# Optimization experiments

Measured on AMD Instinct MI355X. Metric: run time of the kernel, lower is better.

## Reference

```python
import jax, jax.numpy as jnp
import numpy as np

B, D, E, H, T = 16384, 32, 8, 64, 10  # batch, state_dim, n_experts, hidden, time points
TEMP = 1.0  # gating temperature


def setup_inputs() -> dict:
    key = jax.random.key(0)
    ks = jax.random.split(key, 12)
    w = lambda k, shape, fan_in: (jax.random.normal(k, shape, jnp.float32) / np.sqrt(fan_in)).astype(jnp.float32)
    return {
        "x0": jax.random.normal(ks[0], (B, D), jnp.float32),
        "t_span": jnp.linspace(0.0, 1.0, T).astype(jnp.float32),
        # per-expert time-conditioned MLP: (x, t) -> H -> H -> D
        "W1": w(ks[1], (E, D + 1, H), D + 1), "b1": jnp.zeros((E, H), jnp.float32),
        "W2": w(ks[2], (E, H, H), H),          "b2": jnp.zeros((E, H), jnp.float32),
        "W3": w(ks[3], (E, H, D), H),          "b3": jnp.zeros((E, D), jnp.float32),
        # gating MLP on concat(x, dx_init): 2D -> H -> E
        "Gw1": w(ks[4], (2 * D, H), 2 * D), "Gb1": jnp.zeros((H,), jnp.float32),
        "Gw2": w(ks[5], (H, E), H),         "Gb2": jnp.zeros((E,), jnp.float32),
    }


def _dyn(t, x, W1, b1, W2, b2, W3, b3, Gw1, Gb1, Gw2, Gb2):
    # AME-ODE training-path dynamics: uniform-weighted init, gate, weighted sum
    inp = jnp.concatenate([x, jnp.ones((x.shape[0], 1), x.dtype) * t], axis=-1)  # [B, D+1]
    h = jnp.tanh(jnp.einsum('bi,eih->beh', inp, W1) + b1)
    h = jnp.tanh(jnp.einsum('beh,ehg->beg', h, W2) + b2)
    f = jnp.einsum('beg,egd->bed', h, W3) + b3          # all-expert dynamics [B, E, D]
    dx_init = f.mean(axis=1)                             # uniform weights 1/E
    g = jnp.tanh(jnp.concatenate([x, dx_init], -1) @ Gw1 + Gb1)
    wgt = jax.nn.softmax((g @ Gw2 + Gb2) / TEMP, axis=-1)  # [B, E]
    return jnp.einsum('be,bed->bd', wgt, f)


def reference(x0, t_span, W1, b1, W2, b2, W3, b3, Gw1, Gb1, Gw2, Gb2):
    params = (W1, b1, W2, b2, W3, b3, Gw1, Gb1, Gw2, Gb2)

    def step(x, ts):
        t0, t1 = ts[0], ts[1]
        dt = t1 - t0
        k1 = _dyn(t0, x, *params)
        k2 = _dyn(t0 + 0.5 * dt, x + 0.5 * dt * k1, *params)
        k3 = _dyn(t0 + 0.5 * dt, x + 0.5 * dt * k2, *params)
        k4 = _dyn(t1, x + dt * k3, *params)
        xn = x + (dt / 6.0) * (k1 + 2.0 * k2 + 2.0 * k3 + k4)
        return xn, xn

    pairs = jnp.stack([t_span[:-1], t_span[1:]], axis=1)  # [T-1, 2]
    _, traj = jax.lax.scan(step, x0, pairs)               # [T-1, B, D]
    traj = jnp.concatenate([x0[None], traj], axis=0)       # [T, B, D]
    return jnp.transpose(traj, (1, 0, 2))                  # [B, T, D]
```

## Files before the change

kernel.cpp:

```cpp
#include <hip/hip_runtime.h>
#include <hip/hip_bf16.h>

typedef unsigned int u32;
typedef unsigned short u16;
typedef __attribute__((ext_vector_type(8))) short short8;
typedef __attribute__((ext_vector_type(4))) float f32x4;
typedef __attribute__((ext_vector_type(4))) u32 u32x4;
typedef __attribute__((ext_vector_type(2))) u32 u32x2;

#define DD 32
#define EE 8
#define HH 64
#define TT 10
#define BATCH 16384
#define EPB 64
#define DYN_LDS 88064

#if __has_builtin(__builtin_amdgcn_exp2f)
#define EXP2F(x) __builtin_amdgcn_exp2f(x)
#else
#define EXP2F(x) __builtin_exp2f(x)
#endif

__device__ __forceinline__ float fast_tanh(float x) {
  float e = EXP2F(x * 2.885390082f);
  return 1.f - 2.f * __builtin_amdgcn_rcpf(e + 1.f);
}
__device__ __forceinline__ u16 f2b_rn(float v) {
  return (u16)((__float_as_uint(v) + 0x8000u) >> 16);
}
__device__ __forceinline__ u32 pack2_rn(float a, float b) {
  return __builtin_amdgcn_perm(__float_as_uint(b) + 0x8000u,
                               __float_as_uint(a) + 0x8000u, 0x07060302u);
}
__device__ __forceinline__ float unp_lo(u32 p) { return __uint_as_float(p << 16); }
__device__ __forceinline__ float unp_hi(u32 p) { return __uint_as_float(p & 0xffff0000u); }
__device__ __forceinline__ short8 lds_frag(const u32* p) {
  u32x4 v = *(const u32x4*)p;
  return __builtin_bit_cast(short8, v);
}
__device__ __forceinline__ f32x4 bcast4(float v) { f32x4 c; c[0]=v; c[1]=v; c[2]=v; c[3]=v; return c; }

__global__ __launch_bounds__(512) void ame_ode_kernel(
    const float* __restrict__ x0, const float* __restrict__ tspan,
    const float* __restrict__ W1, const float* __restrict__ b1,
    const float* __restrict__ W2, const float* __restrict__ b2,
    const float* __restrict__ W3, const float* __restrict__ b3,
    const float* __restrict__ Gw1, const float* __restrict__ Gb1,
    const float* __restrict__ Gw2, const float* __restrict__ Gb2,
    float* __restrict__ out)
{
  extern __shared__ __align__(16) u32 dynbuf[];
  u32*  const xdb = dynbuf;
  u32*  const fsb = dynbuf + 1280;
  float* const lg = (float*)(dynbuf + 9728);
  u32*  const usb = dynbuf + 10496;
  u32*  const hs  = dynbuf + 12800;

  const int tid  = threadIdx.x;
  const int lane = tid & 63;
  const int l15  = lane & 15;
  const int quad = lane >> 4;
  const int e    = __builtin_amdgcn_readfirstlane(tid >> 6);
  const int b    = blockIdx.x * EPB + lane;

  const float* W1f = W1 + e * (DD + 1) * HH;
  const float* b1f = b1 + e * HH;
  const float* W2f = W2 + e * HH * HH;
  const float* b2f = b2 + e * HH;
  const float* W3f = W3 + e * HH * DD;
  const float* b3f = b3 + e * DD;

  short8 bw1[4], bw2[2][4], bw3[2][2];
  #pragma unroll
  for (int nt = 0; nt < 4; nt++)
    #pragma unroll
    for (int j = 0; j < 8; j++)
      bw1[nt][j] = (short)f2b_rn(W1f[(quad * 8 + j) * HH + nt * 16 + l15]);
  #pragma unroll
  for (int ks = 0; ks < 2; ks++)
    #pragma unroll
    for (int nt = 0; nt < 4; nt++)
      #pragma unroll
      for (int j = 0; j < 8; j++)
        bw2[ks][nt][j] = (short)f2b_rn(W2f[(ks * 32 + quad * 8 + j) * HH + nt * 16 + l15]);
  #pragma unroll
  for (int ks = 0; ks < 2; ks++)
    #pragma unroll
    for (int dt2 = 0; dt2 < 2; dt2++)
      #pragma unroll
      for (int j = 0; j < 8; j++)
        bw3[ks][dt2][j] = (short)f2b_rn(W3f[(ks * 32 + quad * 8 + j) * DD + dt2 * 16 + l15]);

  const int g1mt = e & 3;
  const int g1n0 = (e >> 2) * 2;
  short8 bg1x[2], bg1f[2];
  #pragma unroll
  for (int ni = 0; ni < 2; ni++)
    #pragma unroll
    for (int j = 0; j < 8; j++) {
      bg1x[ni][j] = (short)f2b_rn(Gw1[(quad * 8 + j) * HH + (g1n0 + ni) * 16 + l15]);
      bg1f[ni][j] = (short)f2b_rn(0.125f * Gw1[(DD + quad * 8 + j) * HH + (g1n0 + ni) * 16 + l15]);
    }
  const float gb1a = Gb1[g1n0 * 16 + l15];
  const float gb1b = Gb1[(g1n0 + 1) * 16 + l15];

  short8 bg2[2];
  float gb2v = 0.f;
  if (e < 4) {
    #pragma unroll
    for (int ks = 0; ks < 2; ks++)
      #pragma unroll
      for (int j = 0; j < 8; j++)
        bg2[ks][j] = (short)((l15 < 8) ? f2b_rn(Gw2[(ks * 32 + quad * 8 + j) * EE + l15]) : 0);
    gb2v = (l15 < 8) ? Gb2[l15] : 0.f;
  }

  u32 c1p[4], c2p[2], c3p;
  #pragma unroll
  for (int nt = 0; nt < 4; nt++)
    c1p[nt] = pack2_rn(b1f[nt * 16 + l15], W1f[DD * HH + nt * 16 + l15]);
  #pragma unroll
  for (int p = 0; p < 2; p++)
    c2p[p] = pack2_rn(b2f[(2 * p) * 16 + l15], b2f[(2 * p + 1) * 16 + l15]);
  c3p = pack2_rn(b3f[l15], b3f[16 + l15]);

  float xst[4], xacc[4];
  {
    const float4 v = *(const float4*)(x0 + b * DD + 4 * e);
    xst[0] = v.x; xst[1] = v.y; xst[2] = v.z; xst[3] = v.w;
    xacc[0] = v.x; xacc[1] = v.y; xacc[2] = v.z; xacc[3] = v.w;
    u32x2 p; p.x = pack2_rn(v.x, v.y); p.y = pack2_rn(v.z, v.w);
    *(u32x2*)&xdb[lane * 20 + 2 * e] = p;
    *(float4*)(out + b * TT * DD + 4 * e) = v;
  }
  __syncthreads();

  u16* const fw16 = (u16*)fsb;
  u16* const us16 = (u16*)usb;

  #pragma unroll 1
  for (int step = 0; step < TT - 1; step++) {
    const float t0 = tspan[step];
    const float t1 = tspan[step + 1];
    const float dt = t1 - t0;

    #pragma unroll 1
    for (int s = 0; s < 4; s++) {
      const float tcur = (s == 0) ? t0 : ((s == 3) ? t1 : t0 + 0.5f * dt);

      f32x4 c1i[4];
      #pragma unroll
      for (int nt = 0; nt < 4; nt++)
        c1i[nt] = bcast4(__builtin_fmaf(tcur, unp_hi(c1p[nt]), unp_lo(c1p[nt])));

      #pragma unroll 2
      for (int mt = 0; mt < 4; mt++) {
        u32* const hw   = hs + e * 1152 + (mt & 1) * 576;
        u16* const hw16 = (u16*)hw;

        const short8 a1 = lds_frag(&xdb[(mt * 16 + l15) * 20 + quad * 4]);
        f32x4 h1a[4];
        #pragma unroll
        for (int nt = 0; nt < 4; nt++)
          h1a[nt] = __builtin_amdgcn_mfma_f32_16x16x32_bf16(a1, bw1[nt], c1i[nt], 0, 0, 0);
        #pragma unroll
        for (int nt = 0; nt < 4; nt++)
          #pragma unroll
          for (int r = 0; r < 4; r++)
            hw16[(quad * 4 + r) * 72 + nt * 16 + l15] = f2b_rn(fast_tanh(h1a[nt][r]));

        f32x4 h2a[4];
        #pragma unroll
        for (int nt = 0; nt < 4; nt++)
          h2a[nt] = bcast4((nt & 1) ? unp_hi(c2p[nt >> 1]) : unp_lo(c2p[nt >> 1]));
        #pragma unroll
        for (int ks = 0; ks < 2; ks++) {
          const short8 a2 = lds_frag(&hw[l15 * 36 + ks * 16 + quad * 4]);
          #pragma unroll
          for (int nt = 0; nt < 4; nt++)
            h2a[nt] = __builtin_amdgcn_mfma_f32_16x16x32_bf16(a2, bw2[ks][nt], h2a[nt], 0, 0, 0);
        }
        #pragma unroll
        for (int nt = 0; nt < 4; nt++)
          #pragma unroll
          for (int r = 0; r < 4; r++)
            hw16[(quad * 4 + r) * 72 + nt * 16 + l15] = f2b_rn(fast_tanh(h2a[nt][r]));

        f32x4 fa[2];
        #pragma unroll
        for (int dt2 = 0; dt2 < 2; dt2++)
          fa[dt2] = bcast4(dt2 ? unp_hi(c3p) : unp_lo(c3p));
        #pragma unroll
        for (int ks = 0; ks < 2; ks++) {
          const short8 a3 = lds_frag(&hw[l15 * 36 + ks * 16 + quad * 4]);
          #pragma unroll
          for (int dt2 = 0; dt2 < 2; dt2++)
            fa[dt2] = __builtin_amdgcn_mfma_f32_16x16x32_bf16(a3, bw3[ks][dt2], fa[dt2], 0, 0, 0);
        }
        #pragma unroll
        for (int dt2 = 0; dt2 < 2; dt2++)
          #pragma unroll
          for (int r = 0; r < 4; r++)
            fw16[(mt * 16 + quad * 4 + r) * 264 + e * 32 + dt2 * 16 + l15] = f2b_rn(fa[dt2][r]);
      }
      __syncthreads();

      {
        f32x4 u0 = bcast4(gb1a), u1 = bcast4(gb1b);
        const int mg = g1mt * 16 + l15;
        const short8 ax = lds_frag(&xdb[mg * 20 + quad * 4]);
        u0 = __builtin_amdgcn_mfma_f32_16x16x32_bf16(ax, bg1x[0], u0, 0, 0, 0);
        u1 = __builtin_amdgcn_mfma_f32_16x16x32_bf16(ax, bg1x[1], u1, 0, 0, 0);
        #pragma unroll
        for (int kb = 0; kb < 8; kb++) {
          const short8 af = lds_frag(&fsb[mg * 132 + kb * 16 + quad * 4]);
          u0 = __builtin_amdgcn_mfma_f32_16x16x32_bf16(af, bg1f[0], u0, 0, 0, 0);
          u1 = __builtin_amdgcn_mfma_f32_16x16x32_bf16(af, bg1f[1], u1, 0, 0, 0);
        }
        #pragma unroll
        for (int r = 0; r < 4; r++) {
          us16[(g1mt * 16 + quad * 4 + r) * 72 + g1n0 * 16 + l15]       = f2b_rn(fast_tanh(u0[r]));
          us16[(g1mt * 16 + quad * 4 + r) * 72 + (g1n0 + 1) * 16 + l15] = f2b_rn(fast_tanh(u1[r]));
        }
      }
      __syncthreads();

      if (e < 4) {
        f32x4 lv = bcast4(gb2v);
        #pragma unroll
        for (int ks = 0; ks < 2; ks++) {
          const short8 ag = lds_frag(&usb[(e * 16 + l15) * 36 + ks * 16 + quad * 4]);
          lv = __builtin_amdgcn_mfma_f32_16x16x32_bf16(ag, bg2[ks], lv, 0, 0, 0);
        }
        if (l15 < 8) {
          #pragma unroll
          for (int r = 0; r < 4; r++)
            lg[(e * 16 + quad * 4 + r) * 12 + l15] = lv[r];
        }
      }
      __syncthreads();

      {
        const float4 la0 = *(const float4*)&lg[lane * 12 + 0];
        const float4 la1 = *(const float4*)&lg[lane * 12 + 4];
        float w8[EE];
        w8[0] = __expf(la0.x); w8[1] = __expf(la0.y);
        w8[2] = __expf(la0.z); w8[3] = __expf(la0.w);
        w8[4] = __expf(la1.x); w8[5] = __expf(la1.y);
        w8[6] = __expf(la1.z); w8[7] = __expf(la1.w);
        float ss = 0.f;
        #pragma unroll
        for (int j = 0; j < EE; j++) ss += w8[j];
        const float inv = __builtin_amdgcn_rcpf(ss);

        float kc[4] = {0.f, 0.f, 0.f, 0.f};
        #pragma unroll
        for (int j = 0; j < EE; j++) {
          const float wg = w8[j] * inv;
          const u32x2 p = *(const u32x2*)&fsb[lane * 132 + j * 16 + 2 * e];
          kc[0] = __builtin_fmaf(wg, unp_lo(p.x), kc[0]);
          kc[1] = __builtin_fmaf(wg, unp_hi(p.x), kc[1]);
          kc[2] = __builtin_fmaf(wg, unp_lo(p.y), kc[2]);
          kc[3] = __builtin_fmaf(wg, unp_hi(p.y), kc[3]);
        }

        const float wk = (s == 1 || s == 2) ? 2.f : 1.f;
        const float ak = dt * (1.f / 6.f) * wk;
        #pragma unroll
        for (int q = 0; q < 4; q++) xacc[q] = __builtin_fmaf(ak, kc[q], xacc[q]);

        float xn[4];
        if (s < 3) {
          const float cn = (s == 2) ? dt : 0.5f * dt;
          #pragma unroll
          for (int q = 0; q < 4; q++) xn[q] = __builtin_fmaf(cn, kc[q], xst[q]);
        } else {
          #pragma unroll
          for (int q = 0; q < 4; q++) { xst[q] = xacc[q]; xn[q] = xacc[q]; }
          float4 o; o.x = xn[0]; o.y = xn[1]; o.z = xn[2]; o.w = xn[3];
          *(float4*)(out + (b * TT + step + 1) * DD + 4 * e) = o;
        }
        u32x2 p; p.x = pack2_rn(xn[0], xn[1]); p.y = pack2_rn(xn[2], xn[3]);
        *(u32x2*)&xdb[lane * 20 + 2 * e] = p;
      }
      __syncthreads();
    }
  }
}

extern "C" void kernel_launch(void* const* d_in, const int* in_sizes, int n_in,
                              void* d_out, int out_size, void* d_ws, size_t ws_size,
                              hipStream_t stream)
{
  const float* x0    = (const float*)d_in[0];
  const float* tspan = (const float*)d_in[1];
  const float* W1  = (const float*)d_in[2];
  const float* b1  = (const float*)d_in[3];
  const float* W2  = (const float*)d_in[4];
  const float* b2  = (const float*)d_in[5];
  const float* W3  = (const float*)d_in[6];
  const float* b3  = (const float*)d_in[7];
  const float* Gw1 = (const float*)d_in[8];
  const float* Gb1 = (const float*)d_in[9];
  const float* Gw2 = (const float*)d_in[10];
  const float* Gb2 = (const float*)d_in[11];

  (void)hipFuncSetAttribute((const void*)ame_ode_kernel,
                            hipFuncAttributeMaxDynamicSharedMemorySize, DYN_LDS);

  ame_ode_kernel<<<BATCH / EPB, 512, DYN_LDS, stream>>>(
      x0, tspan, W1, b1, W2, b2, W3, b3, Gw1, Gb1, Gw2, Gb2, (float*)d_out);
}
```

Baseline: 318.4 us.

## Halve batch elements per block to 32 and remap gating and combine work

Reduces the number of batch rows each 512-thread block processes from 64 to 32. This doubles the grid size and shrinks the LDS footprint, so more blocks can be resident on each CU. The gating MLP tiles are remapped so each wave owns one 16x16 output tile, and the combine stage now gives each thread two state elements. Per-block weight loading and bf16 conversion are amortized over half as many rows, and each wave does less MFMA work per barrier, which may expose synchronization overhead.

```diff
diff --git a/kernel.cpp b/kernel.cpp
--- a/kernel.cpp
+++ b/kernel.cpp
@@ -13,8 +13,8 @@
 #define HH 64
 #define TT 10
 #define BATCH 16384
-#define EPB 64
-#define DYN_LDS 88064
+#define EPB 32
+#define DYN_LDS 62464
 
 #if __has_builtin(__builtin_amdgcn_exp2f)
 #define EXP2F(x) __builtin_amdgcn_exp2f(x)
@@ -52,17 +52,20 @@
 {
   extern __shared__ __align__(16) u32 dynbuf[];
   u32*  const xdb = dynbuf;
-  u32*  const fsb = dynbuf + 1280;
-  float* const lg = (float*)(dynbuf + 9728);
-  u32*  const usb = dynbuf + 10496;
-  u32*  const hs  = dynbuf + 12800;
+  u32*  const fsb = dynbuf + 640;
+  float* const lg = (float*)(dynbuf + 4864);
+  u32*  const usb = dynbuf + 5248;
+  u32*  const hs  = dynbuf + 6400;
 
   const int tid  = threadIdx.x;
   const int lane = tid & 63;
   const int l15  = lane & 15;
   const int quad = lane >> 4;
   const int e    = __builtin_amdgcn_readfirstlane(tid >> 6);
-  const int b    = blockIdx.x * EPB + lane;
+
+  const int cm = tid & 31;
+  const int cg = tid >> 5;
+  const int cb = blockIdx.x * EPB + cm;
 
   const float* W1f = W1 + e * (DD + 1) * HH;
   const float* b1f = b1 + e * HH;
@@ -92,22 +95,19 @@
       for (int j = 0; j < 8; j++)
         bw3[ks][dt2][j] = (short)f2b_rn(W3f[(ks * 32 + quad * 8 + j) * DD + dt2 * 16 + l15]);
 
-  const int g1mt = e & 3;
-  const int g1n0 = (e >> 2) * 2;
-  short8 bg1x[2], bg1f[2];
-  #pragma unroll
-  for (int ni = 0; ni < 2; ni++)
-    #pragma unroll
-    for (int j = 0; j < 8; j++) {
-      bg1x[ni][j] = (short)f2b_rn(Gw1[(quad * 8 + j) * HH + (g1n0 + ni) * 16 + l15]);
-      bg1f[ni][j] = (short)f2b_rn(0.125f * Gw1[(DD + quad * 8 + j) * HH + (g1n0 + ni) * 16 + l15]);
-    }
-  const float gb1a = Gb1[g1n0 * 16 + l15];
-  const float gb1b = Gb1[(g1n0 + 1) * 16 + l15];
+  const int g1mt = e & 1;
+  const int g1nt = e >> 1;
+  short8 bg1x, bg1f;
+  #pragma unroll
+  for (int j = 0; j < 8; j++) {
+    bg1x[j] = (short)f2b_rn(Gw1[(quad * 8 + j) * HH + g1nt * 16 + l15]);
+    bg1f[j] = (short)f2b_rn(0.125f * Gw1[(DD + quad * 8 + j) * HH + g1nt * 16 + l15]);
+  }
+  const float gb1a = Gb1[g1nt * 16 + l15];
 
   short8 bg2[2];
   float gb2v = 0.f;
-  if (e < 4) {
+  if (e < 2) {
     #pragma unroll
     for (int ks = 0; ks < 2; ks++)
       #pragma unroll
@@ -125,14 +125,13 @@
     c2p[p] = pack2_rn(b2f[(2 * p) * 16 + l15], b2f[(2 * p + 1) * 16 + l15]);
   c3p = pack2_rn(b3f[l15], b3f[16 + l15]);
 
-  float xst[4], xacc[4];
+  float xst[2], xacc[2];
   {
-    const float4 v = *(const float4*)(x0 + b * DD + 4 * e);
-    xst[0] = v.x; xst[1] = v.y; xst[2] = v.z; xst[3] = v.w;
-    xacc[0] = v.x; xacc[1] = v.y; xacc[2] = v.z; xacc[3] = v.w;
-    u32x2 p; p.x = pack2_rn(v.x, v.y); p.y = pack2_rn(v.z, v.w);
-    *(u32x2*)&xdb[lane * 20 + 2 * e] = p;
-    *(float4*)(out + b * TT * DD + 4 * e) = v;
+    const float2 v = *(const float2*)(x0 + cb * DD + 2 * cg);
+    xst[0] = v.x; xst[1] = v.y;
+    xacc[0] = v.x; xacc[1] = v.y;
+    xdb[cm * 20 + cg] = pack2_rn(v.x, v.y);
+    *(float2*)(out + cb * TT * DD + 2 * cg) = v;
   }
   __syncthreads();
 
@@ -155,7 +154,7 @@
         c1i[nt] = bcast4(__builtin_fmaf(tcur, unp_hi(c1p[nt]), unp_lo(c1p[nt])));
 
       #pragma unroll 2
-      for (int mt = 0; mt < 4; mt++) {
+      for (int mt = 0; mt < 2; mt++) {
         u32* const hw   = hs + e * 1152 + (mt & 1) * 576;
         u16* const hw16 = (u16*)hw;
 
@@ -207,26 +206,22 @@
       __syncthreads();
 
       {
-        f32x4 u0 = bcast4(gb1a), u1 = bcast4(gb1b);
+        f32x4 u0 = bcast4(gb1a);
         const int mg = g1mt * 16 + l15;
         const short8 ax = lds_frag(&xdb[mg * 20 + quad * 4]);
-        u0 = __builtin_amdgcn_mfma_f32_16x16x32_bf16(ax, bg1x[0], u0, 0, 0, 0);
-        u1 = __builtin_amdgcn_mfma_f32_16x16x32_bf16(ax, bg1x[1], u1, 0, 0, 0);
+        u0 = __builtin_amdgcn_mfma_f32_16x16x32_bf16(ax, bg1x, u0, 0, 0, 0);
         #pragma unroll
         for (int kb = 0; kb < 8; kb++) {
           const short8 af = lds_frag(&fsb[mg * 132 + kb * 16 + quad * 4]);
-          u0 = __builtin_amdgcn_mfma_f32_16x16x32_bf16(af, bg1f[0], u0, 0, 0, 0);
-          u1 = __builtin_amdgcn_mfma_f32_16x16x32_bf16(af, bg1f[1], u1, 0, 0, 0);
-        }
-        #pragma unroll
-        for (int r = 0; r < 4; r++) {
-          us16[(g1mt * 16 + quad * 4 + r) * 72 + g1n0 * 16 + l15]       = f2b_rn(fast_tanh(u0[r]));
-          us16[(g1mt * 16 + quad * 4 + r) * 72 + (g1n0 + 1) * 16 + l15] = f2b_rn(fast_tanh(u1[r]));
-        }
+          u0 = __builtin_amdgcn_mfma_f32_16x16x32_bf16(af, bg1f, u0, 0, 0, 0);
+        }
+        #pragma unroll
+        for (int r = 0; r < 4; r++)
+          us16[(g1mt * 16 + quad * 4 + r) * 72 + g1nt * 16 + l15] = f2b_rn(fast_tanh(u0[r]));
       }
       __syncthreads();
 
-      if (e < 4) {
+      if (e < 2) {
         f32x4 lv = bcast4(gb2v);
         #pragma unroll
         for (int ks = 0; ks < 2; ks++) {
@@ -242,8 +237,8 @@
       __syncthreads();
 
       {
-        const float4 la0 = *(const float4*)&lg[lane * 12 + 0];
-        const float4 la1 = *(const float4*)&lg[lane * 12 + 4];
+        const float4 la0 = *(const float4*)&lg[cm * 12 + 0];
+        const float4 la1 = *(const float4*)&lg[cm * 12 + 4];
         float w8[EE];
         w8[0] = __expf(la0.x); w8[1] = __expf(la0.y);
         w8[2] = __expf(la0.z); w8[3] = __expf(la0.w);
@@ -254,35 +249,32 @@
         for (int j = 0; j < EE; j++) ss += w8[j];
         const float inv = __builtin_amdgcn_rcpf(ss);
 
-        float kc[4] = {0.f, 0.f, 0.f, 0.f};
+        float kc[2] = {0.f, 0.f};
         #pragma unroll
         for (int j = 0; j < EE; j++) {
           const float wg = w8[j] * inv;
-          const u32x2 p = *(const u32x2*)&fsb[lane * 132 + j * 16 + 2 * e];
-          kc[0] = __builtin_fmaf(wg, unp_lo(p.x), kc[0]);
-          kc[1] = __builtin_fmaf(wg, unp_hi(p.x), kc[1]);
-          kc[2] = __builtin_fmaf(wg, unp_lo(p.y), kc[2]);
-          kc[3] = __builtin_fmaf(wg, unp_hi(p.y), kc[3]);
+          const u32 p = fsb[cm * 132 + j * 16 + cg];
+          kc[0] = __builtin_fmaf(wg, unp_lo(p), kc[0]);
+          kc[1] = __builtin_fmaf(wg, unp_hi(p), kc[1]);
         }
 
         const float wk = (s == 1 || s == 2) ? 2.f : 1.f;
         const float ak = dt * (1.f / 6.f) * wk;
         #pragma unroll
-        for (int q = 0; q < 4; q++) xacc[q] = __builtin_fmaf(ak, kc[q], xacc[q]);
-
-        float xn[4];
+        for (int q = 0; q < 2; q++) xacc[q] = __builtin_fmaf(ak, kc[q], xacc[q]);
+
+        float xn[2];
         if (s < 3) {
           const float cn = (s == 2) ? dt : 0.5f * dt;
           #pragma unroll
-          for (int q = 0; q < 4; q++) xn[q] = __builtin_fmaf(cn, kc[q], xst[q]);
+          for (int q = 0; q < 2; q++) xn[q] = __builtin_fmaf(cn, kc[q], xst[q]);
         } else {
           #pragma unroll
-          for (int q = 0; q < 4; q++) { xst[q] = xacc[q]; xn[q] = xacc[q]; }
-          float4 o; o.x = xn[0]; o.y = xn[1]; o.z = xn[2]; o.w = xn[3];
-          *(float4*)(out + (b * TT + step + 1) * DD + 4 * e) = o;
-        }
-        u32x2 p; p.x = pack2_rn(xn[0], xn[1]); p.y = pack2_rn(xn[2], xn[3]);
-        *(u32x2*)&xdb[lane * 20 + 2 * e] = p;
+          for (int q = 0; q < 2; q++) { xst[q] = xacc[q]; xn[q] = xacc[q]; }
+          float2 o; o.x = xn[0]; o.y = xn[1];
+          *(float2*)(out + (cb * TT + step + 1) * DD + 2 * cg) = o;
+        }
+        xdb[cm * 20 + cg] = pack2_rn(xn[0], xn[1]);
       }
       __syncthreads();
     }
```

After: 351.8 us. 10.5% more time.

## Give each wave its own 8 batch rows for gating and combine to cut barriers

Applied to the files above, without the earlier changes.

Each wave now owns 8 batch rows for the gating MLP, softmax and RK4 state update, where before each wave owned one slice of the state across all 64 rows. The gate runs inside the wave: it uses 16-row MFMA tiles with the rows duplicated, the logits stay in registers, and the softmax sum is done with lane shuffles. A per-wave LDS scratch hands the weights to the combine step. This removes two block-wide __syncthreads per RK stage and the shared logit and hidden buffers, which also shrinks LDS. In exchange, half of each gating MFMA is redundant work, every wave now runs the gate (before, only four waves did the second layer), and more gating weights stay resident in registers.

```diff
diff --git a/kernel.cpp b/kernel.cpp
--- a/kernel.cpp
+++ b/kernel.cpp
@@ -14,7 +14,7 @@
 #define TT 10
 #define BATCH 16384
 #define EPB 64
-#define DYN_LDS 88064
+#define DYN_LDS 75776
 
 #if __has_builtin(__builtin_amdgcn_exp2f)
 #define EXP2F(x) __builtin_amdgcn_exp2f(x)
@@ -53,16 +53,18 @@
   extern __shared__ __align__(16) u32 dynbuf[];
   u32*  const xdb = dynbuf;
   u32*  const fsb = dynbuf + 1280;
-  float* const lg = (float*)(dynbuf + 9728);
-  u32*  const usb = dynbuf + 10496;
-  u32*  const hs  = dynbuf + 12800;
+  u32*  const hs  = dynbuf + 9728;
 
   const int tid  = threadIdx.x;
   const int lane = tid & 63;
   const int l15  = lane & 15;
   const int quad = lane >> 4;
   const int e    = __builtin_amdgcn_readfirstlane(tid >> 6);
-  const int b    = blockIdx.x * EPB + lane;
+
+  const int el = lane >> 3;
+  const int q8 = lane & 7;
+  const int gr = e * 8 + el;
+  const int gb = blockIdx.x * EPB + gr;
 
   const float* W1f = W1 + e * (DD + 1) * HH;
   const float* b1f = b1 + e * HH;
@@ -92,29 +94,25 @@
       for (int j = 0; j < 8; j++)
         bw3[ks][dt2][j] = (short)f2b_rn(W3f[(ks * 32 + quad * 8 + j) * DD + dt2 * 16 + l15]);
 
-  const int g1mt = e & 3;
-  const int g1n0 = (e >> 2) * 2;
-  short8 bg1x[2], bg1f[2];
-  #pragma unroll
-  for (int ni = 0; ni < 2; ni++)
+  short8 bg1x[4], bg1f[4];
+  float gb1v[4];
+  #pragma unroll
+  for (int nt = 0; nt < 4; nt++) {
     #pragma unroll
     for (int j = 0; j < 8; j++) {
-      bg1x[ni][j] = (short)f2b_rn(Gw1[(quad * 8 + j) * HH + (g1n0 + ni) * 16 + l15]);
-      bg1f[ni][j] = (short)f2b_rn(0.125f * Gw1[(DD + quad * 8 + j) * HH + (g1n0 + ni) * 16 + l15]);
+      bg1x[nt][j] = (short)f2b_rn(Gw1[(quad * 8 + j) * HH + nt * 16 + l15]);
+      bg1f[nt][j] = (short)f2b_rn(0.125f * Gw1[(DD + quad * 8 + j) * HH + nt * 16 + l15]);
     }
-  const float gb1a = Gb1[g1n0 * 16 + l15];
-  const float gb1b = Gb1[(g1n0 + 1) * 16 + l15];
+    gb1v[nt] = Gb1[nt * 16 + l15];
+  }
 
   short8 bg2[2];
-  float gb2v = 0.f;
-  if (e < 4) {
-    #pragma unroll
-    for (int ks = 0; ks < 2; ks++)
-      #pragma unroll
-      for (int j = 0; j < 8; j++)
-        bg2[ks][j] = (short)((l15 < 8) ? f2b_rn(Gw2[(ks * 32 + quad * 8 + j) * EE + l15]) : 0);
-    gb2v = (l15 < 8) ? Gb2[l15] : 0.f;
-  }
+  #pragma unroll
+  for (int ks = 0; ks < 2; ks++)
+    #pragma unroll
+    for (int j = 0; j < 8; j++)
+      bg2[ks][j] = (short)((l15 < 8) ? f2b_rn(Gw2[(ks * 32 + quad * 8 + j) * EE + l15]) : 0);
+  const float gb2v = (l15 < 8) ? Gb2[l15] : 0.f;
 
   u32 c1p[4], c2p[2], c3p;
   #pragma unroll
@@ -127,17 +125,19 @@
 
   float xst[4], xacc[4];
   {
-    const float4 v = *(const float4*)(x0 + b * DD + 4 * e);
+    const float4 v = *(const float4*)(x0 + gb * DD + q8 * 4);
     xst[0] = v.x; xst[1] = v.y; xst[2] = v.z; xst[3] = v.w;
     xacc[0] = v.x; xacc[1] = v.y; xacc[2] = v.z; xacc[3] = v.w;
     u32x2 p; p.x = pack2_rn(v.x, v.y); p.y = pack2_rn(v.z, v.w);
-    *(u32x2*)&xdb[lane * 20 + 2 * e] = p;
-    *(float4*)(out + b * TT * DD + 4 * e) = v;
+    *(u32x2*)&xdb[gr * 20 + q8 * 2] = p;
+    *(float4*)(out + gb * TT * DD + q8 * 4) = v;
   }
   __syncthreads();
 
-  u16* const fw16 = (u16*)fsb;
-  u16* const us16 = (u16*)usb;
+  u16*  const fw16 = (u16*)fsb;
+  u32*  const hsw  = hs + e * 1152;
+  u16*  const uw16 = (u16*)hsw;
+  float* const wscr = (float*)(hsw + 576);
 
   #pragma unroll 1
   for (int step = 0; step < TT - 1; step++) {
@@ -156,7 +156,7 @@
 
       #pragma unroll 2
       for (int mt = 0; mt < 4; mt++) {
-        u32* const hw   = hs + e * 1152 + (mt & 1) * 576;
+        u32* const hw   = hsw + (mt & 1) * 576;
         u16* const hw16 = (u16*)hw;
 
         const short8 a1 = lds_frag(&xdb[(mt * 16 + l15) * 20 + quad * 4]);
@@ -204,86 +204,83 @@
           for (int r = 0; r < 4; r++)
             fw16[(mt * 16 + quad * 4 + r) * 264 + e * 32 + dt2 * 16 + l15] = f2b_rn(fa[dt2][r]);
       }
+
+      f32x4 u4[4];
+      {
+        const short8 ax = lds_frag(&xdb[(e * 8 + (l15 & 7)) * 20 + quad * 4]);
+        #pragma unroll
+        for (int nt = 0; nt < 4; nt++)
+          u4[nt] = __builtin_amdgcn_mfma_f32_16x16x32_bf16(ax, bg1x[nt], bcast4(gb1v[nt]), 0, 0, 0);
+      }
       __syncthreads();
 
-      {
-        f32x4 u0 = bcast4(gb1a), u1 = bcast4(gb1b);
-        const int mg = g1mt * 16 + l15;
-        const short8 ax = lds_frag(&xdb[mg * 20 + quad * 4]);
-        u0 = __builtin_amdgcn_mfma_f32_16x16x32_bf16(ax, bg1x[0], u0, 0, 0, 0);
-        u1 = __builtin_amdgcn_mfma_f32_16x16x32_bf16(ax, bg1x[1], u1, 0, 0, 0);
-        #pragma unroll
-        for (int kb = 0; kb < 8; kb++) {
-          const short8 af = lds_frag(&fsb[mg * 132 + kb * 16 + quad * 4]);
-          u0 = __builtin_amdgcn_mfma_f32_16x16x32_bf16(af, bg1f[0], u0, 0, 0, 0);
-          u1 = __builtin_amdgcn_mfma_f32_16x16x32_bf16(af, bg1f[1], u1, 0, 0, 0);
-        }
-        #pragma unroll
-        for (int r = 0; r < 4; r++) {
-          us16[(g1mt * 16 + quad * 4 + r) * 72 + g1n0 * 16 + l15]       = f2b_rn(fast_tanh(u0[r]));
-          us16[(g1mt * 16 + quad * 4 + r) * 72 + (g1n0 + 1) * 16 + l15] = f2b_rn(fast_tanh(u1[r]));
-        }
-      }
-      __syncthreads();
-
-      if (e < 4) {
-        f32x4 lv = bcast4(gb2v);
-        #pragma unroll
-        for (int ks = 0; ks < 2; ks++) {
-          const short8 ag = lds_frag(&usb[(e * 16 + l15) * 36 + ks * 16 + quad * 4]);
-          lv = __builtin_amdgcn_mfma_f32_16x16x32_bf16(ag, bg2[ks], lv, 0, 0, 0);
-        }
-        if (l15 < 8) {
-          #pragma unroll
-          for (int r = 0; r < 4; r++)
-            lg[(e * 16 + quad * 4 + r) * 12 + l15] = lv[r];
-        }
-      }
-      __syncthreads();
-
-      {
-        const float4 la0 = *(const float4*)&lg[lane * 12 + 0];
-        const float4 la1 = *(const float4*)&lg[lane * 12 + 4];
-        float w8[EE];
-        w8[0] = __expf(la0.x); w8[1] = __expf(la0.y);
-        w8[2] = __expf(la0.z); w8[3] = __expf(la0.w);
-        w8[4] = __expf(la1.x); w8[5] = __expf(la1.y);
-        w8[6] = __expf(la1.z); w8[7] = __expf(la1.w);
-        float ss = 0.f;
-        #pragma unroll
-        for (int j = 0; j < EE; j++) ss += w8[j];
-        const float inv = __builtin_amdgcn_rcpf(ss);
-
-        float kc[4] = {0.f, 0.f, 0.f, 0.f};
-        #pragma unroll
-        for (int j = 0; j < EE; j++) {
-          const float wg = w8[j] * inv;
-          const u32x2 p = *(const u32x2*)&fsb[lane * 132 + j * 16 + 2 * e];
-          kc[0] = __builtin_fmaf(wg, unp_lo(p.x), kc[0]);
-          kc[1] = __builtin_fmaf(wg, unp_hi(p.x), kc[1]);
-          kc[2] = __builtin_fmaf(wg, unp_lo(p.y), kc[2]);
-          kc[3] = __builtin_fmaf(wg, unp_hi(p.y), kc[3]);
-        }
-
-        const float wk = (s == 1 || s == 2) ? 2.f : 1.f;
-        const float ak = dt * (1.f / 6.f) * wk;
-        #pragma unroll
-        for (int q = 0; q < 4; q++) xacc[q] = __builtin_fmaf(ak, kc[q], xacc[q]);
-
-        float xn[4];
-        if (s < 3) {
-          const float cn = (s == 2) ? dt : 0.5f * dt;
-          #pragma unroll
-          for (int q = 0; q < 4; q++) xn[q] = __builtin_fmaf(cn, kc[q], xst[q]);
-        } else {
-          #pragma unroll
-          for (int q = 0; q < 4; q++) { xst[q] = xacc[q]; xn[q] = xacc[q]; }
-          float4 o; o.x = xn[0]; o.y = xn[1]; o.z = xn[2]; o.w = xn[3];
-          *(float4*)(out + (b * TT + step + 1) * DD + 4 * e) = o;
-        }
-        u32x2 p; p.x = pack2_rn(xn[0], xn[1]); p.y = pack2_rn(xn[2], xn[3]);
-        *(u32x2*)&xdb[lane * 20 + 2 * e] = p;
-      }
+      #pragma unroll
+      for (int kb = 0; kb < 8; kb++) {
+        const short8 af = lds_frag(&fsb[(e * 8 + (l15 & 7)) * 132 + kb * 16 + quad * 4]);
+        #pragma unroll
+        for (int nt = 0; nt < 4; nt++)
+          u4[nt] = __builtin_amdgcn_mfma_f32_16x16x32_bf16(af, bg1f[nt], u4[nt], 0, 0, 0);
+      }
+      #pragma unroll
+      for (int nt = 0; nt < 4; nt++)
+        #pragma unroll
+        for (int r = 0; r < 4; r++)
+          uw16[(quad * 4 + r) * 72 + nt * 16 + l15] = f2b_rn(fast_tanh(u4[nt][r]));
+
+      f32x4 lv = bcast4(gb2v);
+      #pragma unroll
+      for (int ks = 0; ks < 2; ks++) {
+        const short8 ag = lds_frag(&hsw[l15 * 36 + ks * 16 + quad * 4]);
+        lv = __builtin_amdgcn_mfma_f32_16x16x32_bf16(ag, bg2[ks], lv, 0, 0, 0);
+      }
+
+      float wgt[4];
+      #pragma unroll
+      for (int r = 0; r < 4; r++) {
+        const float p = __expf(lv[r]);
+        float ssum = p + __shfl_xor(p, 1);
+        ssum += __shfl_xor(ssum, 2);
+        ssum += __shfl_xor(ssum, 4);
+        wgt[r] = p * __builtin_amdgcn_rcpf(ssum);
+      }
+      if (quad < 2 && l15 < 8) {
+        #pragma unroll
+        for (int r = 0; r < 4; r++)
+          wscr[(quad * 4 + r) * 8 + l15] = wgt[r];
+      }
+      const f32x4 w0 = *(const f32x4*)&wscr[el * 8];
+      const f32x4 w1 = *(const f32x4*)&wscr[el * 8 + 4];
+
+      float kc[4] = {0.f, 0.f, 0.f, 0.f};
+      #pragma unroll
+      for (int j = 0; j < EE; j++) {
+        const float wg = (j < 4) ? w0[j] : w1[j - 4];
+        const u32x2 pf = *(const u32x2*)&fsb[gr * 132 + j * 16 + q8 * 2];
+        kc[0] = __builtin_fmaf(wg, unp_lo(pf.x), kc[0]);
+        kc[1] = __builtin_fmaf(wg, unp_hi(pf.x), kc[1]);
+        kc[2] = __builtin_fmaf(wg, unp_lo(pf.y), kc[2]);
+        kc[3] = __builtin_fmaf(wg, unp_hi(pf.y), kc[3]);
+      }
+
+      const float wk = (s == 1 || s == 2) ? 2.f : 1.f;
+      const float ak = dt * (1.f / 6.f) * wk;
+      #pragma unroll
+      for (int q = 0; q < 4; q++) xacc[q] = __builtin_fmaf(ak, kc[q], xacc[q]);
+
+      float xn[4];
+      if (s < 3) {
+        const float cn = (s == 2) ? dt : 0.5f * dt;
+        #pragma unroll
+        for (int q = 0; q < 4; q++) xn[q] = __builtin_fmaf(cn, kc[q], xst[q]);
+      } else {
+        #pragma unroll
+        for (int q = 0; q < 4; q++) { xst[q] = xacc[q]; xn[q] = xacc[q]; }
+        float4 o; o.x = xn[0]; o.y = xn[1]; o.z = xn[2]; o.w = xn[3];
+        *(float4*)(out + (gb * TT + step + 1) * DD + q8 * 4) = o;
+      }
+      u32x2 p; p.x = pack2_rn(xn[0], xn[1]); p.y = pack2_rn(xn[2], xn[3]);
+      *(u32x2*)&xdb[gr * 20 + q8 * 2] = p;
+
       __syncthreads();
     }
   }
```

Result: slower. 343.5 us (+7.9%).

## Swap MFMA operand order to produce transposed tiles with vectorized packed LDS stores

Applied to the files above, without the earlier changes.

All MFMAs now take the weight fragment as A and the activation fragment as B. Each lane therefore holds four consecutive output features for one batch row, so tanh results and f outputs can be packed into bf16 pairs and written with one 8-byte LDS store instead of four scalar 2-byte stores. Because the bias/accumulator init now varies along the lane's four rows, the packed biases and gating biases move from registers into small LDS tables read as vectors. This is meant to cut LDS store instruction count and bank traffic in the inner MLP loop. It adds LDS usage and extra LDS reads for the biases.

```diff
diff --git a/kernel.cpp b/kernel.cpp
--- a/kernel.cpp
+++ b/kernel.cpp
@@ -14,7 +14,7 @@
 #define TT 10
 #define BATCH 16384
 #define EPB 64
-#define DYN_LDS 88064
+#define DYN_LDS 91968
 
 #if __has_builtin(__builtin_amdgcn_exp2f)
 #define EXP2F(x) __builtin_amdgcn_exp2f(x)
@@ -39,7 +39,6 @@
   u32x4 v = *(const u32x4*)p;
   return __builtin_bit_cast(short8, v);
 }
-__device__ __forceinline__ f32x4 bcast4(float v) { f32x4 c; c[0]=v; c[1]=v; c[2]=v; c[3]=v; return c; }
 
 __global__ __launch_bounds__(512) void ame_ode_kernel(
     const float* __restrict__ x0, const float* __restrict__ tspan,
@@ -51,11 +50,16 @@
     float* __restrict__ out)
 {
   extern __shared__ __align__(16) u32 dynbuf[];
-  u32*  const xdb = dynbuf;
-  u32*  const fsb = dynbuf + 1280;
-  float* const lg = (float*)(dynbuf + 9728);
-  u32*  const usb = dynbuf + 10496;
-  u32*  const hs  = dynbuf + 12800;
+  u32*  const xdb  = dynbuf;
+  u32*  const fsb  = dynbuf + 1280;
+  float* const lg  = (float*)(dynbuf + 9728);
+  u32*  const ust  = dynbuf + 10496;
+  u32*  const hs   = dynbuf + 12800;
+  u32*  const cb1  = dynbuf + 22016;
+  u32*  const cb2  = dynbuf + 22528;
+  u32*  const cb3  = dynbuf + 22784;
+  float* const gb1s = (float*)(dynbuf + 22912);
+  float* const gb2s = (float*)(dynbuf + 22976);
 
   const int tid  = threadIdx.x;
   const int lane = tid & 63;
@@ -102,28 +106,26 @@
       bg1x[ni][j] = (short)f2b_rn(Gw1[(quad * 8 + j) * HH + (g1n0 + ni) * 16 + l15]);
       bg1f[ni][j] = (short)f2b_rn(0.125f * Gw1[(DD + quad * 8 + j) * HH + (g1n0 + ni) * 16 + l15]);
     }
-  const float gb1a = Gb1[g1n0 * 16 + l15];
-  const float gb1b = Gb1[(g1n0 + 1) * 16 + l15];
 
   short8 bg2[2];
-  float gb2v = 0.f;
   if (e < 4) {
     #pragma unroll
     for (int ks = 0; ks < 2; ks++)
       #pragma unroll
       for (int j = 0; j < 8; j++)
         bg2[ks][j] = (short)((l15 < 8) ? f2b_rn(Gw2[(ks * 32 + quad * 8 + j) * EE + l15]) : 0);
-    gb2v = (l15 < 8) ? Gb2[l15] : 0.f;
   }
 
-  u32 c1p[4], c2p[2], c3p;
-  #pragma unroll
-  for (int nt = 0; nt < 4; nt++)
-    c1p[nt] = pack2_rn(b1f[nt * 16 + l15], W1f[DD * HH + nt * 16 + l15]);
-  #pragma unroll
-  for (int p = 0; p < 2; p++)
-    c2p[p] = pack2_rn(b2f[(2 * p) * 16 + l15], b2f[(2 * p + 1) * 16 + l15]);
-  c3p = pack2_rn(b3f[l15], b3f[16 + l15]);
+  {
+    u32* const c1e = cb1 + e * 64;
+    c1e[lane] = pack2_rn(b1f[lane], W1f[DD * HH + lane]);
+    if (lane < 32) (cb2 + e * 32)[lane] = pack2_rn(b2f[2 * lane], b2f[2 * lane + 1]);
+    if (lane < 16) (cb3 + e * 16)[lane] = pack2_rn(b3f[2 * lane], b3f[2 * lane + 1]);
+    if (e == 0) {
+      gb1s[lane] = Gb1[lane];
+      if (lane < 16) gb2s[lane] = (lane < 8) ? Gb2[lane] : 0.f;
+    }
+  }
 
   float xst[4], xacc[4];
   {
@@ -136,8 +138,12 @@
   }
   __syncthreads();
 
-  u16* const fw16 = (u16*)fsb;
-  u16* const us16 = (u16*)usb;
+  u16* const fw16  = (u16*)fsb;
+  u32* const hsw   = hs + e * 1152;
+  u16* const ust16 = (u16*)ust;
+  const u32* const c1e = cb1 + e * 64;
+  const u32* const c2e = cb2 + e * 32;
+  const u32* const c3e = cb3 + e * 16;
 
   #pragma unroll 1
   for (int step = 0; step < TT - 1; step++) {
@@ -151,92 +157,117 @@
 
       f32x4 c1i[4];
       #pragma unroll
-      for (int nt = 0; nt < 4; nt++)
-        c1i[nt] = bcast4(__builtin_fmaf(tcur, unp_hi(c1p[nt]), unp_lo(c1p[nt])));
+      for (int nt = 0; nt < 4; nt++) {
+        const u32x4 cw = *(const u32x4*)&c1e[nt * 16 + quad * 4];
+        c1i[nt][0] = __builtin_fmaf(tcur, unp_hi(cw[0]), unp_lo(cw[0]));
+        c1i[nt][1] = __builtin_fmaf(tcur, unp_hi(cw[1]), unp_lo(cw[1]));
+        c1i[nt][2] = __builtin_fmaf(tcur, unp_hi(cw[2]), unp_lo(cw[2]));
+        c1i[nt][3] = __builtin_fmaf(tcur, unp_hi(cw[3]), unp_lo(cw[3]));
+      }
 
       #pragma unroll 2
       for (int mt = 0; mt < 4; mt++) {
-        u32* const hw   = hs + e * 1152 + (mt & 1) * 576;
-        u16* const hw16 = (u16*)hw;
+        u32* const hT32 = hsw + (mt & 1) * 576;
+        u16* const hT16 = (u16*)hT32;
 
         const short8 a1 = lds_frag(&xdb[(mt * 16 + l15) * 20 + quad * 4]);
         f32x4 h1a[4];
         #pragma unroll
         for (int nt = 0; nt < 4; nt++)
-          h1a[nt] = __builtin_amdgcn_mfma_f32_16x16x32_bf16(a1, bw1[nt], c1i[nt], 0, 0, 0);
+          h1a[nt] = __builtin_amdgcn_mfma_f32_16x16x32_bf16(bw1[nt], a1, c1i[nt], 0, 0, 0);
+        #pragma unroll
+        for (int nt = 0; nt < 4; nt++) {
+          u32x2 pw;
+          pw.x = pack2_rn(fast_tanh(h1a[nt][0]), fast_tanh(h1a[nt][1]));
+          pw.y = pack2_rn(fast_tanh(h1a[nt][2]), fast_tanh(h1a[nt][3]));
+          *(u32x2*)&hT16[l15 * 72 + nt * 16 + quad * 4] = pw;
+        }
+
+        f32x4 h2a[4];
+        #pragma unroll
+        for (int nt = 0; nt < 4; nt++) {
+          const u32x2 cw = *(const u32x2*)&c2e[nt * 8 + quad * 2];
+          h2a[nt][0] = unp_lo(cw.x); h2a[nt][1] = unp_hi(cw.x);
+          h2a[nt][2] = unp_lo(cw.y); h2a[nt][3] = unp_hi(cw.y);
+        }
+        const short8 a2k0 = lds_frag(&hT32[l15 * 36 + quad * 4]);
+        const short8 a2k1 = lds_frag(&hT32[l15 * 36 + 16 + quad * 4]);
         #pragma unroll
         for (int nt = 0; nt < 4; nt++)
-          #pragma unroll
-          for (int r = 0; r < 4; r++)
-            hw16[(quad * 4 + r) * 72 + nt * 16 + l15] = f2b_rn(fast_tanh(h1a[nt][r]));
-
-        f32x4 h2a[4];
+          h2a[nt] = __builtin_amdgcn_mfma_f32_16x16x32_bf16(bw2[0][nt], a2k0, h2a[nt], 0, 0, 0);
         #pragma unroll
         for (int nt = 0; nt < 4; nt++)
-          h2a[nt] = bcast4((nt & 1) ? unp_hi(c2p[nt >> 1]) : unp_lo(c2p[nt >> 1]));
-        #pragma unroll
-        for (int ks = 0; ks < 2; ks++) {
-          const short8 a2 = lds_frag(&hw[l15 * 36 + ks * 16 + quad * 4]);
-          #pragma unroll
-          for (int nt = 0; nt < 4; nt++)
-            h2a[nt] = __builtin_amdgcn_mfma_f32_16x16x32_bf16(a2, bw2[ks][nt], h2a[nt], 0, 0, 0);
-        }
-        #pragma unroll
-        for (int nt = 0; nt < 4; nt++)
-          #pragma unroll
-          for (int r = 0; r < 4; r++)
-            hw16[(quad * 4 + r) * 72 + nt * 16 + l15] = f2b_rn(fast_tanh(h2a[nt][r]));
+          h2a[nt] = __builtin_amdgcn_mfma_f32_16x16x32_bf16(bw2[1][nt], a2k1, h2a[nt], 0, 0, 0);
+        #pragma unroll
+        for (int nt = 0; nt < 4; nt++) {
+          u32x2 pw;
+          pw.x = pack2_rn(fast_tanh(h2a[nt][0]), fast_tanh(h2a[nt][1]));
+          pw.y = pack2_rn(fast_tanh(h2a[nt][2]), fast_tanh(h2a[nt][3]));
+          *(u32x2*)&hT16[l15 * 72 + nt * 16 + quad * 4] = pw;
+        }
 
         f32x4 fa[2];
         #pragma unroll
+        for (int dt2 = 0; dt2 < 2; dt2++) {
+          const u32x2 cw = *(const u32x2*)&c3e[dt2 * 8 + quad * 2];
+          fa[dt2][0] = unp_lo(cw.x); fa[dt2][1] = unp_hi(cw.x);
+          fa[dt2][2] = unp_lo(cw.y); fa[dt2][3] = unp_hi(cw.y);
+        }
+        const short8 a3k0 = lds_frag(&hT32[l15 * 36 + quad * 4]);
+        const short8 a3k1 = lds_frag(&hT32[l15 * 36 + 16 + quad * 4]);
+        #pragma unroll
         for (int dt2 = 0; dt2 < 2; dt2++)
-          fa[dt2] = bcast4(dt2 ? unp_hi(c3p) : unp_lo(c3p));
-        #pragma unroll
-        for (int ks = 0; ks < 2; ks++) {
-          const short8 a3 = lds_frag(&hw[l15 * 36 + ks * 16 + quad * 4]);
-          #pragma unroll
-          for (int dt2 = 0; dt2 < 2; dt2++)
-            fa[dt2] = __builtin_amdgcn_mfma_f32_16x16x32_bf16(a3, bw3[ks][dt2], fa[dt2], 0, 0, 0);
-        }
+          fa[dt2] = __builtin_amdgcn_mfma_f32_16x16x32_bf16(bw3[0][dt2], a3k0, fa[dt2], 0, 0, 0);
         #pragma unroll
         for (int dt2 = 0; dt2 < 2; dt2++)
-          #pragma unroll
-          for (int r = 0; r < 4; r++)
-            fw16[(mt * 16 + quad * 4 + r) * 264 + e * 32 + dt2 * 16 + l15] = f2b_rn(fa[dt2][r]);
+          fa[dt2] = __builtin_amdgcn_mfma_f32_16x16x32_bf16(bw3[1][dt2], a3k1, fa[dt2], 0, 0, 0);
+        #pragma unroll
+        for (int dt2 = 0; dt2 < 2; dt2++) {
+          u32x2 pw;
+          pw.x = pack2_rn(fa[dt2][0], fa[dt2][1]);
+          pw.y = pack2_rn(fa[dt2][2], fa[dt2][3]);
+          *(u32x2*)&fw16[(mt * 16 + l15) * 264 + e * 32 + dt2 * 16 + quad * 4] = pw;
+        }
       }
       __syncthreads();
 
       {
-        f32x4 u0 = bcast4(gb1a), u1 = bcast4(gb1b);
+        f32x4 ug[2];
+        #pragma unroll
+        for (int mi = 0; mi < 2; mi++) {
+          const float4 gbv = *(const float4*)&gb1s[(g1n0 + mi) * 16 + quad * 4];
+          ug[mi][0] = gbv.x; ug[mi][1] = gbv.y; ug[mi][2] = gbv.z; ug[mi][3] = gbv.w;
+        }
         const int mg = g1mt * 16 + l15;
-        const short8 ax = lds_frag(&xdb[mg * 20 + quad * 4]);
-        u0 = __builtin_amdgcn_mfma_f32_16x16x32_bf16(ax, bg1x[0], u0, 0, 0, 0);
-        u1 = __builtin_amdgcn_mfma_f32_16x16x32_bf16(ax, bg1x[1], u1, 0, 0, 0);
+        const short8 bx = lds_frag(&xdb[mg * 20 + quad * 4]);
+        ug[0] = __builtin_amdgcn_mfma_f32_16x16x32_bf16(bg1x[0], bx, ug[0], 0, 0, 0);
+        ug[1] = __builtin_amdgcn_mfma_f32_16x16x32_bf16(bg1x[1], bx, ug[1], 0, 0, 0);
         #pragma unroll
         for (int kb = 0; kb < 8; kb++) {
-          const short8 af = lds_frag(&fsb[mg * 132 + kb * 16 + quad * 4]);
-          u0 = __builtin_amdgcn_mfma_f32_16x16x32_bf16(af, bg1f[0], u0, 0, 0, 0);
-          u1 = __builtin_amdgcn_mfma_f32_16x16x32_bf16(af, bg1f[1], u1, 0, 0, 0);
-        }
-        #pragma unroll
-        for (int r = 0; r < 4; r++) {
-          us16[(g1mt * 16 + quad * 4 + r) * 72 + g1n0 * 16 + l15]       = f2b_rn(fast_tanh(u0[r]));
-          us16[(g1mt * 16 + quad * 4 + r) * 72 + (g1n0 + 1) * 16 + l15] = f2b_rn(fast_tanh(u1[r]));
+          const short8 bf = lds_frag(&fsb[mg * 132 + kb * 16 + quad * 4]);
+          ug[0] = __builtin_amdgcn_mfma_f32_16x16x32_bf16(bg1f[0], bf, ug[0], 0, 0, 0);
+          ug[1] = __builtin_amdgcn_mfma_f32_16x16x32_bf16(bg1f[1], bf, ug[1], 0, 0, 0);
+        }
+        #pragma unroll
+        for (int mi = 0; mi < 2; mi++) {
+          u32x2 pw;
+          pw.x = pack2_rn(fast_tanh(ug[mi][0]), fast_tanh(ug[mi][1]));
+          pw.y = pack2_rn(fast_tanh(ug[mi][2]), fast_tanh(ug[mi][3]));
+          *(u32x2*)&ust16[mg * 72 + (g1n0 + mi) * 16 + quad * 4] = pw;
         }
       }
       __syncthreads();
 
       if (e < 4) {
-        f32x4 lv = bcast4(gb2v);
-        #pragma unroll
-        for (int ks = 0; ks < 2; ks++) {
-          const short8 ag = lds_frag(&usb[(e * 16 + l15) * 36 + ks * 16 + quad * 4]);
-          lv = __builtin_amdgcn_mfma_f32_16x16x32_bf16(ag, bg2[ks], lv, 0, 0, 0);
-        }
-        if (l15 < 8) {
-          #pragma unroll
-          for (int r = 0; r < 4; r++)
-            lg[(e * 16 + quad * 4 + r) * 12 + l15] = lv[r];
+        const float4 g2b = *(const float4*)&gb2s[quad * 4];
+        f32x4 lv; lv[0] = g2b.x; lv[1] = g2b.y; lv[2] = g2b.z; lv[3] = g2b.w;
+        const short8 bu0 = lds_frag(&ust[(e * 16 + l15) * 36 + quad * 4]);
+        const short8 bu1 = lds_frag(&ust[(e * 16 + l15) * 36 + 16 + quad * 4]);
+        lv = __builtin_amdgcn_mfma_f32_16x16x32_bf16(bg2[0], bu0, lv, 0, 0, 0);
+        lv = __builtin_amdgcn_mfma_f32_16x16x32_bf16(bg2[1], bu1, lv, 0, 0, 0);
+        if (quad < 2) {
+          float4 o; o.x = lv[0]; o.y = lv[1]; o.z = lv[2]; o.w = lv[3];
+          *(float4*)&lg[(e * 16 + l15) * 12 + quad * 4] = o;
         }
       }
       __syncthreads();
```

Result: slower. 334.4 us (+5.0%).
